# Kernel tuning notes

Hardware: AMD Instinct MI355X
Metric: run time of the kernel (lower is better)

Reference implementation:

```python
import jax, jax.numpy as jnp
import numpy as np

TEMPERATURE = 0.1


def setup_inputs() -> dict:
    key = jax.random.key(0)
    k1, k2 = jax.random.split(key)
    N, D = 8192, 128
    features = jax.random.normal(k1, (N, D), dtype=jnp.float32)
    labels = jax.random.randint(k2, (N,), 0, 1000, dtype=jnp.int64)
    return {"features": features, "labels": labels}


def reference(features, labels):
    N = features.shape[0]
    # L2-normalize rows
    feats = features / jnp.linalg.norm(features, axis=1, keepdims=True)
    # positive-pair mask from labels [N, N]
    labels = labels.reshape(-1, 1)
    mask = (labels == labels.T).astype(feats.dtype)
    # similarity matrix scaled by temperature
    sim = jnp.matmul(feats, feats.T) / TEMPERATURE
    # exclude self-comparisons (diagonal)
    logits_mask = 1.0 - jnp.eye(N, dtype=feats.dtype)
    mask = mask * logits_mask
    exp_logits = jnp.exp(sim) * logits_mask
    log_prob = sim - jnp.log(exp_logits.sum(axis=1, keepdims=True) + 1e-9)
    mask_sum = mask.sum(axis=1)
    mask_sum = jnp.where(mask_sum == 0, jnp.ones_like(mask_sum), mask_sum)
    mean_log_prob_pos = (mask * log_prob).sum(axis=1) / mask_sum
    return -mean_log_prob_pos.mean()
```

## Files before the change

### kernel.cpp

```cpp
#include <hip/hip_runtime.h>
#include <hip/hip_bf16.h>
#include <math.h>


constexpr int N = 8192;
constexpr int D = 128;

typedef __attribute__((ext_vector_type(8))) short short8;
typedef __attribute__((ext_vector_type(4))) float f32x4;

__device__ __forceinline__ float fast_exp2(float x) {
#if __has_builtin(__builtin_amdgcn_exp2f)
    return __builtin_amdgcn_exp2f(x);
#else
    return __expf(x * 0.69314718056f);
#endif
}

__device__ __forceinline__ void gload_lds16(const void* g, void* s) {
    __builtin_amdgcn_global_load_lds(
        (const __attribute__((address_space(1))) unsigned int*)g,
        (__attribute__((address_space(3))) unsigned int*)s, 16, 0, 0);
}

__device__ __forceinline__ void stage_tile(const unsigned short* __restrict__ src,
                                           unsigned short* dst, int row0,
                                           int w, int lr, int lq) {
#pragma unroll
    for (int it = 0; it < 8; ++it) {
        int rbase = w * 32 + it * 4;
        int r = rbase + lr;
        int q = lq ^ (r & 7);
        gload_lds16(src + ((size_t)(row0 + r) * D + q * 8), dst + rbase * D);
    }
}

__global__ void prep_kernel(const float* __restrict__ F,
                            unsigned short* __restrict__ Fb,
                            float* __restrict__ rowExp,
                            float* __restrict__ rowPos) {
    int row = blockIdx.x * 4 + (threadIdx.x >> 6);
    int l = threadIdx.x & 63;
    float2 v = ((const float2*)(F + (size_t)row * D))[l];
    float ss = v.x * v.x + v.y * v.y;
#pragma unroll
    for (int off = 32; off > 0; off >>= 1) ss += __shfl_xor(ss, off);
    float sc = sqrtf(14.4269504089f / ss);
    __hip_bfloat16 hx = __float2bfloat16(v.x * sc);
    __hip_bfloat16 hy = __float2bfloat16(v.y * sc);
    ushort2 u;
    u.x = *(unsigned short*)&hx;
    u.y = *(unsigned short*)&hy;
    ((ushort2*)(Fb + (size_t)row * D))[l] = u;
    if (l == 0) {
        rowExp[row] = 0.0f;
        rowPos[row] = 0.0f;
    }
}

__global__ __launch_bounds__(256, 2) void sim_kernel(
    const unsigned short* __restrict__ Fb, const int* __restrict__ labels,
    float* __restrict__ rowExp, float* __restrict__ rowPos) {
    __shared__ unsigned short At[128 * D];
    __shared__ unsigned short Bt[128 * D];

    int bid = blockIdx.x, q = 0, base = 0;
    while (bid >= base + 4 * (16 - q)) { base += 4 * (16 - q); ++q; }
    int rem = bid - base, ng = 16 - q;
    int ti = 4 * q + rem / ng;
    int g = 15 - (rem % ng);
    int tjs = max(ti, 4 * g), tje = 4 * g + 3;
    const int i0 = ti * 128;

    const int t = threadIdx.x, w = t >> 6, l = t & 63;
    const int lr = l >> 4, lq = l & 15;
    const int c = l & 15, quad = l >> 4;
    const int wy = w >> 1, wx = w & 1;

    stage_tile(Fb, At, i0, w, lr, lq);
    stage_tile(Fb, Bt, tjs * 128, w, lr, lq);

    int li[4][4];
#pragma unroll
    for (int m = 0; m < 4; ++m)
#pragma unroll
        for (int r = 0; r < 4; ++r)
            li[m][r] = labels[i0 + wy * 64 + m * 16 + quad * 4 + r];

    float RE[4][4] = {}, RP[4][4] = {};

    for (int tj = tjs; tj <= tje; ++tj) {
        __syncthreads();
        int j0 = tj * 128;
        f32x4 acc[4][4] = {};
#pragma unroll
        for (int kk = 0; kk < 4; ++kk) {
            short8 af[4], bf[4];
            int sl = (kk * 4 + quad) ^ (c & 7);
#pragma unroll
            for (int m = 0; m < 4; ++m) {
                af[m] = *(const short8*)&At[(wy * 64 + m * 16 + c) * D + sl * 8];
                bf[m] = *(const short8*)&Bt[(wx * 64 + m * 16 + c) * D + sl * 8];
            }
#pragma unroll
            for (int m = 0; m < 4; ++m)
#pragma unroll
                for (int n = 0; n < 4; ++n)
                    acc[m][n] = __builtin_amdgcn_mfma_f32_16x16x32_bf16(
                        af[m], bf[n], acc[m][n], 0, 0, 0);
        }
        __syncthreads();
        if (tj < tje) stage_tile(Fb, Bt, (tj + 1) * 128, w, lr, lq);

        int lj[4];
#pragma unroll
        for (int n = 0; n < 4; ++n) lj[n] = labels[j0 + wx * 64 + n * 16 + c];

        if (tj == ti) {
#pragma unroll
            for (int m = 0; m < 4; ++m) {
#pragma unroll
                for (int n = 0; n < 4; ++n) {
#pragma unroll
                    for (int r = 0; r < 4; ++r) {
                        float s2 = acc[m][n][r];
                        bool self = (wy * 64 + m * 16 + quad * 4 + r) ==
                                    (wx * 64 + n * 16 + c);
                        float e = self ? 0.0f : fast_exp2(s2);
                        float p = (!self && li[m][r] == lj[n]) ? s2 : 0.0f;
                        RE[m][r] += e;
                        RP[m][r] += p;
                    }
                }
            }
        } else {
            float ce[4] = {}, cp[4] = {};
#pragma unroll
            for (int m = 0; m < 4; ++m) {
#pragma unroll
                for (int n = 0; n < 4; ++n) {
#pragma unroll
                    for (int r = 0; r < 4; ++r) {
                        float s2 = acc[m][n][r];
                        float e = fast_exp2(s2);
                        float p = (li[m][r] == lj[n]) ? s2 : 0.0f;
                        RE[m][r] += e;
                        RP[m][r] += p;
                        ce[n] += e;
                        cp[n] += p;
                    }
                }
            }
#pragma unroll
            for (int n = 0; n < 4; ++n) {
                ce[n] += __shfl_xor(ce[n], 16);
                ce[n] += __shfl_xor(ce[n], 32);
                cp[n] += __shfl_xor(cp[n], 16);
                cp[n] += __shfl_xor(cp[n], 32);
            }
            if (quad == 0) {
#pragma unroll
                for (int n = 0; n < 4; ++n) {
                    int gj = j0 + wx * 64 + n * 16 + c;
                    atomicAdd(&rowExp[gj], ce[n]);
                    atomicAdd(&rowPos[gj], cp[n]);
                }
            }
        }
    }

#pragma unroll
    for (int m = 0; m < 4; ++m)
#pragma unroll
        for (int r = 0; r < 4; ++r) {
#pragma unroll
            for (int off = 1; off < 16; off <<= 1) {
                RE[m][r] += __shfl_xor(RE[m][r], off);
                RP[m][r] += __shfl_xor(RP[m][r], off);
            }
        }
    if (c == 0) {
#pragma unroll
        for (int m = 0; m < 4; ++m)
#pragma unroll
            for (int r = 0; r < 4; ++r) {
                int gi = i0 + wy * 64 + m * 16 + quad * 4 + r;
                atomicAdd(&rowExp[gi], RE[m][r]);
                atomicAdd(&rowPos[gi], RP[m][r]);
            }
    }
}

__global__ void finalize_kernel(const float* __restrict__ rowExp,
                                const float* __restrict__ rowPos,
                                const int* __restrict__ labels,
                                float* __restrict__ out) {
    __shared__ int hist[1024];
    __shared__ float ws16[16];
    int t = threadIdx.x;
    hist[t] = 0;
    __syncthreads();
    int lab[8];
#pragma unroll
    for (int k = 0; k < 8; ++k) {
        lab[k] = labels[t + 1024 * k];
        atomicAdd(&hist[lab[k]], 1);
    }
    __syncthreads();
    float a = 0.0f;
#pragma unroll
    for (int k = 0; k < 8; ++k) {
        int i = t + 1024 * k;
        int cnt = hist[lab[k]] - 1;
        if (cnt > 0)
            a += logf(rowExp[i] + 1e-9f) -
                 0.69314718056f * rowPos[i] / (float)cnt;
    }
#pragma unroll
    for (int off = 32; off > 0; off >>= 1) a += __shfl_xor(a, off);
    if ((t & 63) == 0) ws16[t >> 6] = a;
    __syncthreads();
    if (t == 0) {
        float s = 0.0f;
#pragma unroll
        for (int i = 0; i < 16; ++i) s += ws16[i];
        out[0] = s / (float)N;
    }
}

extern "C" void kernel_launch(void* const* d_in, const int* in_sizes, int n_in,
                              void* d_out, int out_size, void* d_ws, size_t ws_size,
                              hipStream_t stream) {
    const float* F      = (const float*)d_in[0];
    const int*   labels = (const int*)d_in[1];
    float* out = (float*)d_out;

    unsigned short* Fb = (unsigned short*)d_ws;
    float* rowExp = (float*)(Fb + (size_t)N * D);
    float* rowPos = rowExp + N;

    prep_kernel<<<N / 4, 256, 0, stream>>>(F, Fb, rowExp, rowPos);
    sim_kernel<<<544, 256, 0, stream>>>(Fb, labels, rowExp, rowPos);
    finalize_kernel<<<1, 1024, 0, stream>>>(rowExp, rowPos, labels, out);
}
```

Baseline: 115.5 us.

## Compute full similarity matrix instead of exploiting symmetry

```diff
diff --git a/kernel.cpp b/kernel.cpp
--- a/kernel.cpp
+++ b/kernel.cpp
@@ -64,12 +64,9 @@
     __shared__ unsigned short At[128 * D];
     __shared__ unsigned short Bt[128 * D];
 
-    int bid = blockIdx.x, q = 0, base = 0;
-    while (bid >= base + 4 * (16 - q)) { base += 4 * (16 - q); ++q; }
-    int rem = bid - base, ng = 16 - q;
-    int ti = 4 * q + rem / ng;
-    int g = 15 - (rem % ng);
-    int tjs = max(ti, 4 * g), tje = 4 * g + 3;
+    const int ti = blockIdx.x >> 4;
+    const int g  = blockIdx.x & 15;
+    const int tjs = g * 4;
     const int i0 = ti * 128;
 
     const int t = threadIdx.x, w = t >> 6, l = t & 63;
@@ -89,9 +86,13 @@
 
     float RE[4][4] = {}, RP[4][4] = {};
 
-    for (int tj = tjs; tj <= tje; ++tj) {
+    for (int tj = tjs; tj < tjs + 4; ++tj) {
         __syncthreads();
-        int j0 = tj * 128;
+        const int j0 = tj * 128;
+        int lj[4];
+#pragma unroll
+        for (int n = 0; n < 4; ++n) lj[n] = labels[j0 + wx * 64 + n * 16 + c];
+
         f32x4 acc[4][4] = {};
 #pragma unroll
         for (int kk = 0; kk < 4; ++kk) {
@@ -110,60 +111,22 @@
                         af[m], bf[n], acc[m][n], 0, 0, 0);
         }
         __syncthreads();
-        if (tj < tje) stage_tile(Fb, Bt, (tj + 1) * 128, w, lr, lq);
-
-        int lj[4];
-#pragma unroll
-        for (int n = 0; n < 4; ++n) lj[n] = labels[j0 + wx * 64 + n * 16 + c];
-
-        if (tj == ti) {
-#pragma unroll
-            for (int m = 0; m < 4; ++m) {
-#pragma unroll
-                for (int n = 0; n < 4; ++n) {
-#pragma unroll
-                    for (int r = 0; r < 4; ++r) {
-                        float s2 = acc[m][n][r];
-                        bool self = (wy * 64 + m * 16 + quad * 4 + r) ==
-                                    (wx * 64 + n * 16 + c);
-                        float e = self ? 0.0f : fast_exp2(s2);
-                        float p = (!self && li[m][r] == lj[n]) ? s2 : 0.0f;
-                        RE[m][r] += e;
-                        RP[m][r] += p;
-                    }
-                }
-            }
-        } else {
-            float ce[4] = {}, cp[4] = {};
-#pragma unroll
-            for (int m = 0; m < 4; ++m) {
-#pragma unroll
-                for (int n = 0; n < 4; ++n) {
-#pragma unroll
-                    for (int r = 0; r < 4; ++r) {
-                        float s2 = acc[m][n][r];
-                        float e = fast_exp2(s2);
-                        float p = (li[m][r] == lj[n]) ? s2 : 0.0f;
-                        RE[m][r] += e;
-                        RP[m][r] += p;
-                        ce[n] += e;
-                        cp[n] += p;
-                    }
-                }
-            }
+        if (tj < tjs + 3) stage_tile(Fb, Bt, (tj + 1) * 128, w, lr, lq);
+
+        const bool diag = (tj == ti);
+#pragma unroll
+        for (int m = 0; m < 4; ++m) {
 #pragma unroll
             for (int n = 0; n < 4; ++n) {
-                ce[n] += __shfl_xor(ce[n], 16);
-                ce[n] += __shfl_xor(ce[n], 32);
-                cp[n] += __shfl_xor(cp[n], 16);
-                cp[n] += __shfl_xor(cp[n], 32);
-            }
-            if (quad == 0) {
-#pragma unroll
-                for (int n = 0; n < 4; ++n) {
-                    int gj = j0 + wx * 64 + n * 16 + c;
-                    atomicAdd(&rowExp[gj], ce[n]);
-                    atomicAdd(&rowPos[gj], cp[n]);
+#pragma unroll
+                for (int r = 0; r < 4; ++r) {
+                    float s2 = acc[m][n][r];
+                    bool self = diag && ((wy * 64 + m * 16 + quad * 4 + r) ==
+                                         (wx * 64 + n * 16 + c));
+                    float e = self ? 0.0f : fast_exp2(s2);
+                    float p = (!self && li[m][r] == lj[n]) ? s2 : 0.0f;
+                    RE[m][r] += e;
+                    RP[m][r] += p;
                 }
             }
         }
@@ -240,6 +203,6 @@
     float* rowPos = rowExp + N;
 
     prep_kernel<<<N / 4, 256, 0, stream>>>(F, Fb, rowExp, rowPos);
-    sim_kernel<<<544, 256, 0, stream>>>(Fb, labels, rowExp, rowPos);
+    sim_kernel<<<64 * 16, 256, 0, stream>>>(Fb, labels, rowExp, rowPos);
     finalize_kernel<<<1, 1024, 0, stream>>>(rowExp, rowPos, labels, out);
 }
```

Result: faster. 106.9 us (-7.4%).
